# Performance work log

Hardware: AMD Instinct MI355X
Metric: run time of the kernel (lower is better)

The kernel has to match this reference:

```python
import jax, jax.numpy as jnp
import numpy as np

T, N, E = 8, 10000, 200000
F_IN, H, OUT = 32, 128, 64
EPS = 1e-5


def setup_inputs() -> dict:
    key = jax.random.key(0)
    ks = jax.random.split(key, 28)
    inp = {}
    inp['x'] = jax.random.normal(ks[0], (T, N, F_IN), jnp.float32)
    inp['edge_index'] = jax.random.randint(ks[1], (2, E), 0, N, dtype=jnp.int32)
    # GCN layer weights (Glorot-ish scale)
    inp['w_gcn0'] = jax.random.normal(ks[2], (F_IN, H), jnp.float32) / np.float32(np.sqrt(F_IN))
    inp['b_gcn0'] = jnp.zeros((H,), jnp.float32)
    inp['w_gcn1'] = jax.random.normal(ks[3], (H, H), jnp.float32) / np.float32(np.sqrt(H))
    inp['b_gcn1'] = jnp.zeros((H,), jnp.float32)
    inp['w_gcn2'] = jax.random.normal(ks[4], (H, H), jnp.float32) / np.float32(np.sqrt(H))
    inp['b_gcn2'] = jnp.zeros((H,), jnp.float32)
    # BatchNorm (eval mode) params for the two inner norms
    for i, kb in zip(range(2), range(5, 9, 2)):
        inp[f'bn_g{i}'] = 1.0 + 0.1 * jax.random.normal(ks[kb], (H,), jnp.float32)
        inp[f'bn_b{i}'] = 0.1 * jax.random.normal(ks[kb + 1], (H,), jnp.float32)
        inp[f'bn_m{i}'] = 0.1 * jax.random.normal(ks[kb + 10], (H,), jnp.float32)
        inp[f'bn_v{i}'] = jax.random.uniform(ks[kb + 11], (H,), jnp.float32, 0.5, 1.5)
    # 3-layer LSTM params, torch gate order (i, f, g, o)
    s = np.float32(1.0 / np.sqrt(OUT))
    dims_in = [H, OUT, OUT]
    for l in range(3):
        k0, k1, k2, k3 = jax.random.split(ks[20 + l], 4)
        inp[f'w_ih_{l}'] = jax.random.uniform(k0, (4 * OUT, dims_in[l]), jnp.float32, -s, s)
        inp[f'w_hh_{l}'] = jax.random.uniform(k1, (4 * OUT, OUT), jnp.float32, -s, s)
        inp[f'b_ih_{l}'] = jax.random.uniform(k2, (4 * OUT,), jnp.float32, -s, s)
        inp[f'b_hh_{l}'] = jax.random.uniform(k3, (4 * OUT,), jnp.float32, -s, s)
    return inp


def reference(x, edge_index, w_gcn0, b_gcn0, w_gcn1, b_gcn1, w_gcn2, b_gcn2,
              bn_g0, bn_b0, bn_m0, bn_v0, bn_g1, bn_b1, bn_m1, bn_v1,
              w_ih_0, w_hh_0, b_ih_0, b_hh_0,
              w_ih_1, w_hh_1, b_ih_1, b_hh_1,
              w_ih_2, w_hh_2, b_ih_2, b_hh_2):
    src, dst = edge_index[0], edge_index[1]
    # symmetric GCN normalization with self-loops: deg = in-degree + 1
    deg = jax.ops.segment_sum(jnp.ones((E,), x.dtype), dst, num_segments=N) + 1.0
    dis = jax.lax.rsqrt(deg)
    coef = dis[src] * dis[dst]          # [E] edge norm
    self_w = dis * dis                   # [N] self-loop norm

    def gcn(h, W, b):
        hw = jnp.einsum('tnf,fo->tno', h, W)                      # [T,N,O]
        msg = hw[:, src, :] * coef[None, :, None]                  # [T,E,O]
        agg = jax.vmap(lambda m: jax.ops.segment_sum(m, dst, num_segments=N))(msg)
        return agg + hw * self_w[None, :, None] + b

    def bn(h, g, b_, m, v):  # eval-mode BatchNorm1d
        return (h - m) * (g * jax.lax.rsqrt(v + EPS)) + b_

    h = bn(jax.nn.relu(gcn(x, w_gcn0, b_gcn0)), bn_g0, bn_b0, bn_m0, bn_v0)
    h = bn(jax.nn.relu(gcn(h, w_gcn1, b_gcn1)), bn_g1, bn_b1, bn_m1, bn_v1)
    h = jax.nn.relu(gcn(h, w_gcn2, b_gcn2))                        # [T,N,H]

    def lstm_layer(xs, Wih, Whh, bih, bhh):
        Hd = Whh.shape[1]
        bias = bih + bhh
        def step(carry, xt):
            hp, cp = carry
            g = xt @ Wih.T + hp @ Whh.T + bias
            i, f, gg, o = jnp.split(g, 4, axis=-1)
            c = jax.nn.sigmoid(f) * cp + jax.nn.sigmoid(i) * jnp.tanh(gg)
            hn = jax.nn.sigmoid(o) * jnp.tanh(c)
            return (hn, c), hn
        z = jnp.zeros((xs.shape[1], Hd), xs.dtype)
        _, ys = jax.lax.scan(step, (z, z), xs)
        return ys  # [T,N,Hd]

    ys = lstm_layer(h, w_ih_0, w_hh_0, b_ih_0, b_hh_0)
    ys = lstm_layer(ys, w_ih_1, w_hh_1, b_ih_1, b_hh_1)
    ys = lstm_layer(ys, w_ih_2, w_hh_2, b_ih_2, b_hh_2)
    return ys[-1]  # [N, OUT] == x[:, -1, :] in the torch code
```

## Files before the change

kernel.cpp:

```cpp
#include <hip/hip_runtime.h>
#include <hip/hip_bf16.h>
#include <math.h>

#define NTHREADS 256
#define T_STEPS 8
#define F_INC 32
#define H_DIM 128
#define O_DIM 64

typedef unsigned short u16;
typedef __attribute__((ext_vector_type(8))) short short8_t;
typedef __attribute__((ext_vector_type(4))) float float4_t;

__device__ __forceinline__ float bf2f(u16 u) {
    return __uint_as_float(((unsigned)u) << 16);
}
__device__ __forceinline__ u16 f2bf(float f) {
    __hip_bfloat16 h = __float2bfloat16(f);
    union { __hip_bfloat16 h; u16 s; } cv; cv.h = h; return cv.s;
}
__device__ __forceinline__ float4 ld_bf4(const u16* p) {
    uint2 u = *(const uint2*)p;
    return make_float4(__uint_as_float(u.x << 16), __uint_as_float(u.x & 0xffff0000u),
                       __uint_as_float(u.y << 16), __uint_as_float(u.y & 0xffff0000u));
}
__device__ __forceinline__ void st_bf4(u16* p, float4 v) {
    ushort4 s = make_ushort4(f2bf(v.x), f2bf(v.y), f2bf(v.z), f2bf(v.w));
    *(ushort4*)p = s;
}
__device__ __forceinline__ void bf8_unpack(uint4 u, float* f) {
    f[0] = __uint_as_float(u.x << 16); f[1] = __uint_as_float(u.x & 0xffff0000u);
    f[2] = __uint_as_float(u.y << 16); f[3] = __uint_as_float(u.y & 0xffff0000u);
    f[4] = __uint_as_float(u.z << 16); f[5] = __uint_as_float(u.z & 0xffff0000u);
    f[6] = __uint_as_float(u.w << 16); f[7] = __uint_as_float(u.w & 0xffff0000u);
}
__device__ __forceinline__ float fsig(float x) {
    float xc = fminf(fmaxf(x, -30.f), 30.f);
    float e = __builtin_amdgcn_exp2f(xc * -1.4426950408889634f);
    return __builtin_amdgcn_rcpf(1.0f + e);
}
__device__ __forceinline__ float ftanh(float x) {
    float xc = fminf(fmaxf(x, -15.f), 15.f);
    float e = __builtin_amdgcn_exp2f(xc * -2.8853900817779268f);
    float r = __builtin_amdgcn_rcpf(1.0f + e);
    return fmaf(-2.0f * e, r, 1.0f);
}

__global__ void init_cnt_kernel(int* __restrict__ cnt, int n) {
    int i = blockIdx.x * NTHREADS + threadIdx.x;
    if (i < n) cnt[i] = 0;
}

__global__ void count_kernel(const int* __restrict__ ei, int* __restrict__ cnt, int E) {
    int e = blockIdx.x * NTHREADS + threadIdx.x;
    if (e < E) atomicAdd(&cnt[ei[E + e]], 1);
}

__global__ void scan_part1(const int* __restrict__ cnt, int* __restrict__ bsum, int n) {
    __shared__ int sd[NTHREADS];
    const int i = blockIdx.x * NTHREADS + threadIdx.x;
    sd[threadIdx.x] = (i < n) ? cnt[i] : 0;
    __syncthreads();
    for (int off = 128; off > 0; off >>= 1) {
        if (threadIdx.x < off) sd[threadIdx.x] += sd[threadIdx.x + off];
        __syncthreads();
    }
    if (threadIdx.x == 0) bsum[blockIdx.x] = sd[0];
}
__global__ void scan_part2(const int* __restrict__ bsum, int* __restrict__ boff, int nb) {
    if (threadIdx.x == 0) {
        int s = 0;
        for (int b = 0; b < nb; ++b) { boff[b] = s; s += bsum[b]; }
    }
}
__global__ void scan_part3(const int* __restrict__ cnt, const int* __restrict__ boff,
                           int* __restrict__ rowptr, int* __restrict__ wp,
                           float* __restrict__ dis, float* __restrict__ selfw, int n) {
    __shared__ int sd[NTHREADS];
    const int i = blockIdx.x * NTHREADS + threadIdx.x;
    const int v = (i < n) ? cnt[i] : 0;
    sd[threadIdx.x] = v;
    __syncthreads();
    for (int off = 1; off < NTHREADS; off <<= 1) {
        const int tv = (threadIdx.x >= off) ? sd[threadIdx.x - off] : 0;
        __syncthreads();
        sd[threadIdx.x] += tv;
        __syncthreads();
    }
    const int excl = boff[blockIdx.x] + sd[threadIdx.x] - v;
    if (i < n) {
        rowptr[i] = excl; wp[i] = excl;
        if (i == n - 1) rowptr[n] = excl + v;
        const float d = 1.0f + (float)v;
        dis[i] = rsqrtf(d);
        selfw[i] = 1.0f / d;
    }
}

__global__ void fill_kernel(const int* __restrict__ ei, const float* __restrict__ dis,
                            int* __restrict__ wp, int* __restrict__ csr_src,
                            float* __restrict__ coefA, int E) {
    int e = blockIdx.x * NTHREADS + threadIdx.x;
    if (e < E) {
        int s = ei[e], d = ei[E + e];
        int p = atomicAdd(&wp[d], 1);
        csr_src[p] = s;
        coefA[p] = dis[s] * dis[d];
    }
}

__global__ void wprep_all_kernel(const float* g0, const float* g1, const float* g2,
                                 const float* i0, const float* i1, const float* i2,
                                 const float* h0, const float* h1, const float* h2,
                                 u16* o_g0, u16* o_g1, u16* o_g2,
                                 u16* o_i0, u16* o_i1, u16* o_i2,
                                 u16* o_h0, u16* o_h1, u16* o_h2) {
    const int i = blockIdx.x * NTHREADS + threadIdx.x;
    if (i < 4096)        { o_g0[i] = f2bf(g0[(i & 31) * 128 + (i >> 5)]); }
    else if (i < 20480)  { int j = i - 4096;   o_g1[j] = f2bf(g1[(j & 127) * 128 + (j >> 7)]); }
    else if (i < 36864)  { int j = i - 20480;  o_g2[j] = f2bf(g2[(j & 127) * 128 + (j >> 7)]); }
    else if (i < 69632)  { int j = i - 36864;  o_i0[j] = f2bf(i0[j]); }
    else if (i < 86016)  { int j = i - 69632;  o_i1[j] = f2bf(i1[j]); }
    else if (i < 102400) { int j = i - 86016;  o_i2[j] = f2bf(i2[j]); }
    else if (i < 118784) { int j = i - 102400; o_h0[j] = f2bf(h0[j]); }
    else if (i < 135168) { int j = i - 118784; o_h1[j] = f2bf(h1[j]); }
    else if (i < 151552) { int j = i - 135168; o_h2[j] = f2bf(h2[j]); }
}

__global__ __launch_bounds__(NTHREADS)
void agg32t_kernel(const float* __restrict__ x, const int* __restrict__ rowptr,
                   const int* __restrict__ csrc, const float* __restrict__ coefA,
                   const float* __restrict__ selfw, u16* __restrict__ out, int N) {
    const int t = blockIdx.x;
    const int n = blockIdx.y * 4 + (threadIdx.x >> 6);
    const int lane = threadIdx.x & 63;
    const int split = lane >> 3;
    const int c4 = (lane & 7) * 4;
    const float* xb = x + (long)t * N * 32;
    const int e0 = rowptr[n], e1 = rowptr[n + 1];
    float a[4] = {};
    #pragma unroll 2
    for (int e = e0 + split; e < e1; e += 8) {
        const float wgt = coefA[e];
        const int s = csrc[e];
        const float4 v = *(const float4*)(xb + (long)s * 32 + c4);
        a[0] = fmaf(wgt, v.x, a[0]);
        a[1] = fmaf(wgt, v.y, a[1]);
        a[2] = fmaf(wgt, v.z, a[2]);
        a[3] = fmaf(wgt, v.w, a[3]);
    }
    #pragma unroll
    for (int j = 0; j < 4; ++j) {
        a[j] += __shfl_xor(a[j], 8);
        a[j] += __shfl_xor(a[j], 16);
        a[j] += __shfl_xor(a[j], 32);
    }
    if (split == 0) {
        const float sw = selfw[n];
        const float4 sv = *(const float4*)(xb + (long)n * 32 + c4);
        float4 r = make_float4(fmaf(sw, sv.x, a[0]), fmaf(sw, sv.y, a[1]),
                               fmaf(sw, sv.z, a[2]), fmaf(sw, sv.w, a[3]));
        st_bf4(out + ((long)t * N + n) * 32 + c4, r);
    }
}

__global__ __launch_bounds__(NTHREADS)
void agg128t_kernel(const u16* __restrict__ h, const int* __restrict__ rowptr,
                    const int* __restrict__ csrc, const float* __restrict__ coefA,
                    const float* __restrict__ selfw, u16* __restrict__ out, int N) {
    const int t = blockIdx.x;
    const int n = blockIdx.y * 4 + (threadIdx.x >> 6);
    const int lane = threadIdx.x & 63;
    const int split = lane >> 4;
    const int c8 = (lane & 15) * 8;
    const u16* hb = h + (long)t * N * 128;
    const int e0 = rowptr[n], e1 = rowptr[n + 1];
    float a[8] = {};
    #pragma unroll 2
    for (int e = e0 + split; e < e1; e += 4) {
        const float wgt = coefA[e];
        const int s = csrc[e];
        const uint4 v = *(const uint4*)(hb + (long)s * 128 + c8);
        float f[8];
        bf8_unpack(v, f);
        #pragma unroll
        for (int j = 0; j < 8; ++j) a[j] = fmaf(wgt, f[j], a[j]);
    }
    #pragma unroll
    for (int j = 0; j < 8; ++j) {
        a[j] += __shfl_xor(a[j], 16);
        a[j] += __shfl_xor(a[j], 32);
    }
    if (split == 0) {
        const float sw = selfw[n];
        const uint4 sv = *(const uint4*)(hb + (long)n * 128 + c8);
        float f[8];
        bf8_unpack(sv, f);
        ushort4 o0, o1;
        o0.x = f2bf(fmaf(sw, f[0], a[0])); o0.y = f2bf(fmaf(sw, f[1], a[1]));
        o0.z = f2bf(fmaf(sw, f[2], a[2])); o0.w = f2bf(fmaf(sw, f[3], a[3]));
        o1.x = f2bf(fmaf(sw, f[4], a[4])); o1.y = f2bf(fmaf(sw, f[5], a[5]));
        o1.z = f2bf(fmaf(sw, f[6], a[6])); o1.w = f2bf(fmaf(sw, f[7], a[7]));
        u16* op = out + ((long)t * N + n) * 128 + c8;
        *(ushort4*)op = o0;
        *(ushort4*)(op + 4) = o1;
    }
}

template<int K, int EPI, bool OUTBF>
__global__ __launch_bounds__(NTHREADS)
void mfma_gemm_kernel(const u16* __restrict__ A, const u16* __restrict__ Bt,
                      const float* __restrict__ bias0,
                      const float* __restrict__ bng, const float* __restrict__ bnb,
                      const float* __restrict__ bnm, const float* __restrict__ bnv,
                      void* __restrict__ Cout, int ldc) {
    constexpr int KC = (K < 64) ? K : 64;
    constexpr int KP = KC + 8;
    constexpr int KV = KC / 8;
    __shared__ __align__(16) u16 As[128 * KP];
    __shared__ __align__(16) u16 Bs[128 * KP];
    const int tid = threadIdx.x;
    const long row0 = (long)blockIdx.x * 128;
    const int col0 = blockIdx.y * 128;
    const int wid = tid >> 6, lane = tid & 63;
    const int quad = lane >> 4, l16 = lane & 15;

    float4_t acc[2][8];
    #pragma unroll
    for (int rt = 0; rt < 2; ++rt)
        #pragma unroll
        for (int ct = 0; ct < 8; ++ct)
            acc[rt][ct] = (float4_t){0.f, 0.f, 0.f, 0.f};

    const int arow = wid * 32 + l16;
    const int koff = quad * 8;
    for (int ch = 0; ch < K / KC; ++ch) {
        const int kbase = ch * KC;
        for (int p = tid; p < 128 * KV; p += NTHREADS) {
            const int r = p / KV, kv = p % KV;
            *(uint4*)(&As[r * KP + kv * 8]) =
                *(const uint4*)(A + (row0 + r) * K + kbase + kv * 8);
        }
        for (int p = tid; p < 128 * KV; p += NTHREADS) {
            const int r = p / KV, kv = p % KV;
            *(uint4*)(&Bs[r * KP + kv * 8]) =
                *(const uint4*)(Bt + (long)(col0 + r) * K + kbase + kv * 8);
        }
        __syncthreads();
        #pragma unroll
        for (int kc = 0; kc < KC / 32; ++kc) {
            const short8_t a0 = *(const short8_t*)(&As[arow * KP + kc * 32 + koff]);
            const short8_t a1 = *(const short8_t*)(&As[(arow + 16) * KP + kc * 32 + koff]);
            #pragma unroll
            for (int ct = 0; ct < 8; ++ct) {
                const short8_t b = *(const short8_t*)(&Bs[(ct * 16 + l16) * KP + kc * 32 + koff]);
                acc[0][ct] = __builtin_amdgcn_mfma_f32_16x16x32_bf16(a0, b, acc[0][ct], 0, 0, 0);
                acc[1][ct] = __builtin_amdgcn_mfma_f32_16x16x32_bf16(a1, b, acc[1][ct], 0, 0, 0);
            }
        }
        __syncthreads();
    }

    float e_add0[8], e_mul[8], e_add1[8];
    #pragma unroll
    for (int ct = 0; ct < 8; ++ct) {
        const int c = col0 + ct * 16 + l16;
        e_add0[ct] = bias0[c];
        if constexpr (EPI == 2) {
            const float s = bng[c] * rsqrtf(bnv[c] + 1e-5f);
            e_mul[ct] = s;
            e_add1[ct] = bnb[c] - bnm[c] * s;
        }
    }
    #pragma unroll
    for (int rt = 0; rt < 2; ++rt) {
        #pragma unroll
        for (int r = 0; r < 4; ++r) {
            const long row = row0 + wid * 32 + rt * 16 + quad * 4 + r;
            #pragma unroll
            for (int ct = 0; ct < 8; ++ct) {
                float v = fmaxf(acc[rt][ct][r] + e_add0[ct], 0.f);
                if constexpr (EPI == 2) v = fmaf(v, e_mul[ct], e_add1[ct]);
                const long idx = row * (long)ldc + col0 + ct * 16 + l16;
                if constexpr (OUTBF) ((u16*)Cout)[idx] = f2bf(v);
                else ((float*)Cout)[idx] = v;
            }
        }
    }
}

template<int KIN, bool IN_SPLIT, bool LAST>
__global__ __launch_bounds__(NTHREADS, 2)
void lstm_layer_kernel(const u16* __restrict__ in_hi, const u16* __restrict__ in_lo,
                       const u16* __restrict__ wih, const u16* __restrict__ whh,
                       const float* __restrict__ bi, const float* __restrict__ bh,
                       u16* __restrict__ out_hi, u16* __restrict__ out_lo,
                       float* __restrict__ out_f, int N) {
    constexpr int NKS = KIN / 32;
    constexpr int HSTR = 76;
    const int tid = threadIdx.x;
    const int w = tid >> 6, lane = tid & 63;
    const int quad = lane >> 4, l16 = lane & 15;
    const int n0 = blockIdx.x * 16;
    const int u = w * 16 + l16;

    __shared__ __align__(16) u16 hT[2][16][HSTR];
    for (int p = tid; p < 2 * 16 * HSTR; p += NTHREADS) (&hT[0][0][0])[p] = 0;

    short8_t fI[4][NKS], fH[4][2];
    #pragma unroll
    for (int g = 0; g < 4; ++g) {
        #pragma unroll
        for (int ks = 0; ks < NKS; ++ks)
            fI[g][ks] = *(const short8_t*)(wih + (long)(g * 64 + u) * KIN + ks * 32 + quad * 8);
        #pragma unroll
        for (int ks = 0; ks < 2; ++ks)
            fH[g][ks] = *(const short8_t*)(whh + (long)(g * 64 + u) * 64 + ks * 32 + quad * 8);
    }
    float bias[4];
    #pragma unroll
    for (int g = 0; g < 4; ++g) bias[g] = bi[g * 64 + u] + bh[g * 64 + u];
    float cst[4] = {};
    __syncthreads();

    #pragma unroll 1
    for (int t = 0; t < T_STEPS; ++t) {
        short8_t ain[NKS], ainl[NKS];
        const long ibase = ((long)t * N + n0 + l16) * KIN + quad * 8;
        #pragma unroll
        for (int ks = 0; ks < NKS; ++ks) {
            ain[ks] = *(const short8_t*)(in_hi + ibase + ks * 32);
            if constexpr (IN_SPLIT) ainl[ks] = *(const short8_t*)(in_lo + ibase + ks * 32);
        }
        short8_t ah[2], al[2];
        #pragma unroll
        for (int ks = 0; ks < 2; ++ks) {
            ah[ks] = *(const short8_t*)(&hT[0][l16][ks * 32 + quad * 8]);
            al[ks] = *(const short8_t*)(&hT[1][l16][ks * 32 + quad * 8]);
        }
        __syncthreads();

        float4_t acc[4];
        #pragma unroll
        for (int g = 0; g < 4; ++g) acc[g] = (float4_t){bias[g], bias[g], bias[g], bias[g]};
        #pragma unroll
        for (int ks = 0; ks < NKS; ++ks)
            #pragma unroll
            for (int g = 0; g < 4; ++g) {
                acc[g] = __builtin_amdgcn_mfma_f32_16x16x32_bf16(ain[ks], fI[g][ks], acc[g], 0, 0, 0);
                if constexpr (IN_SPLIT)
                    acc[g] = __builtin_amdgcn_mfma_f32_16x16x32_bf16(ainl[ks], fI[g][ks], acc[g], 0, 0, 0);
            }
        #pragma unroll
        for (int ks = 0; ks < 2; ++ks)
            #pragma unroll
            for (int g = 0; g < 4; ++g) {
                acc[g] = __builtin_amdgcn_mfma_f32_16x16x32_bf16(ah[ks], fH[g][ks], acc[g], 0, 0, 0);
                acc[g] = __builtin_amdgcn_mfma_f32_16x16x32_bf16(al[ks], fH[g][ks], acc[g], 0, 0, 0);
            }

        #pragma unroll
        for (int r = 0; r < 4; ++r) {
            const float si = fsig(acc[0][r]);
            const float sf = fsig(acc[1][r]);
            const float gg = ftanh(acc[2][r]);
            const float so = fsig(acc[3][r]);
            const float c = sf * cst[r] + si * gg;
            cst[r] = c;
            const float h = so * ftanh(c);
            const int node = quad * 4 + r;
            const u16 hi = f2bf(h);
            const u16 lo = f2bf(h - bf2f(hi));
            hT[0][node][u] = hi;
            hT[1][node][u] = lo;
            if constexpr (LAST) {
                if (t == T_STEPS - 1) out_f[(long)(n0 + node) * 64 + u] = h;
            } else {
                const long o = ((long)t * N + n0 + node) * 64 + u;
                out_hi[o] = hi;
                out_lo[o] = lo;
            }
        }
        __syncthreads();
    }
}

extern "C" void kernel_launch(void* const* d_in, const int* in_sizes, int n_in,
                              void* d_out, int out_size, void* d_ws, size_t ws_size,
                              hipStream_t stream) {
    (void)n_in; (void)out_size; (void)ws_size;
    const float* x      = (const float*)d_in[0];
    const int*   ei     = (const int*)d_in[1];
    const float* w_gcn0 = (const float*)d_in[2];
    const float* b_gcn0 = (const float*)d_in[3];
    const float* w_gcn1 = (const float*)d_in[4];
    const float* b_gcn1 = (const float*)d_in[5];
    const float* w_gcn2 = (const float*)d_in[6];
    const float* b_gcn2 = (const float*)d_in[7];
    const float* bn_g0  = (const float*)d_in[8];
    const float* bn_b0  = (const float*)d_in[9];
    const float* bn_m0  = (const float*)d_in[10];
    const float* bn_v0  = (const float*)d_in[11];
    const float* bn_g1  = (const float*)d_in[12];
    const float* bn_b1  = (const float*)d_in[13];
    const float* bn_m1  = (const float*)d_in[14];
    const float* bn_v1  = (const float*)d_in[15];
    const float* w_ih_0 = (const float*)d_in[16];
    const float* w_hh_0 = (const float*)d_in[17];
    const float* b_ih_0 = (const float*)d_in[18];
    const float* b_hh_0 = (const float*)d_in[19];
    const float* w_ih_1 = (const float*)d_in[20];
    const float* w_hh_1 = (const float*)d_in[21];
    const float* b_ih_1 = (const float*)d_in[22];
    const float* b_hh_1 = (const float*)d_in[23];
    const float* w_ih_2 = (const float*)d_in[24];
    const float* w_hh_2 = (const float*)d_in[25];
    const float* b_ih_2 = (const float*)d_in[26];
    const float* b_hh_2 = (const float*)d_in[27];

    const int E = in_sizes[1] / 2;
    const int N = in_sizes[0] / (T_STEPS * F_INC);
    const long M = (long)N * T_STEPS;

    char* ws = (char*)d_ws;
    size_t off = 0;
    auto carve = [&](size_t bytes) -> void* {
        void* p = ws + off;
        off += (bytes + 255) & ~(size_t)255;
        return p;
    };
    float* dis     = (float*)carve((size_t)N * 4);
    float* selfw   = (float*)carve((size_t)N * 4);
    float* coefA   = (float*)carve((size_t)E * 4);
    int*   cnt     = (int*)carve((size_t)N * 4);
    int*   rowptr  = (int*)carve((size_t)(N + 1) * 4);
    int*   wp      = (int*)carve((size_t)N * 4);
    int*   csr_src = (int*)carve((size_t)E * 4);
    int*   bsum    = (int*)carve(64 * 4);
    int*   boff    = (int*)carve(64 * 4);
    u16*   hbuf    = (u16*)carve((size_t)M * H_DIM * 2);
    u16*   abuf    = (u16*)carve((size_t)M * H_DIM * 2);
    u16*   pA_hi   = (u16*)carve((size_t)M * O_DIM * 2);
    u16*   pA_lo   = (u16*)carve((size_t)M * O_DIM * 2);
    u16*   pB_hi   = (u16*)carve((size_t)M * O_DIM * 2);
    u16*   pB_lo   = (u16*)carve((size_t)M * O_DIM * 2);
    u16*   wt0     = (u16*)carve((size_t)128 * 32 * 2);
    u16*   wt1     = (u16*)carve((size_t)128 * 128 * 2);
    u16*   wt2     = (u16*)carve((size_t)128 * 128 * 2);
    u16*   wtih0   = (u16*)carve((size_t)256 * 128 * 2);
    u16*   wtih1   = (u16*)carve((size_t)256 * 64 * 2);
    u16*   wtih2   = (u16*)carve((size_t)256 * 64 * 2);
    u16*   whh0b   = (u16*)carve((size_t)256 * 64 * 2);
    u16*   whh1b   = (u16*)carve((size_t)256 * 64 * 2);
    u16*   whh2b   = (u16*)carve((size_t)256 * 64 * 2);

    const dim3 b256(NTHREADS);
    const int gN = (N + NTHREADS - 1) / NTHREADS;
    const int gE = (E + NTHREADS - 1) / NTHREADS;

    init_cnt_kernel<<<gN, b256, 0, stream>>>(cnt, N);
    count_kernel<<<gE, b256, 0, stream>>>(ei, cnt, E);
    scan_part1<<<gN, b256, 0, stream>>>(cnt, bsum, N);
    scan_part2<<<1, 64, 0, stream>>>(bsum, boff, gN);
    scan_part3<<<gN, b256, 0, stream>>>(cnt, boff, rowptr, wp, dis, selfw, N);
    fill_kernel<<<gE, b256, 0, stream>>>(ei, dis, wp, csr_src, coefA, E);

    wprep_all_kernel<<<(151552 + 255) / 256, b256, 0, stream>>>(
        w_gcn0, w_gcn1, w_gcn2, w_ih_0, w_ih_1, w_ih_2, w_hh_0, w_hh_1, w_hh_2,
        wt0, wt1, wt2, wtih0, wtih1, wtih2, whh0b, whh1b, whh2b);

    const int gBlk = (int)(M / 128);
    agg32t_kernel<<<dim3(T_STEPS, N / 4), b256, 0, stream>>>(
        x, rowptr, csr_src, coefA, selfw, abuf, N);
    mfma_gemm_kernel<32, 2, true><<<dim3(gBlk, 1), b256, 0, stream>>>(
        abuf, wt0, b_gcn0, bn_g0, bn_b0, bn_m0, bn_v0, hbuf, 128);
    agg128t_kernel<<<dim3(T_STEPS, N / 4), b256, 0, stream>>>(
        hbuf, rowptr, csr_src, coefA, selfw, abuf, N);
    mfma_gemm_kernel<128, 2, true><<<dim3(gBlk, 1), b256, 0, stream>>>(
        abuf, wt1, b_gcn1, bn_g1, bn_b1, bn_m1, bn_v1, hbuf, 128);
    agg128t_kernel<<<dim3(T_STEPS, N / 4), b256, 0, stream>>>(
        hbuf, rowptr, csr_src, coefA, selfw, abuf, N);
    mfma_gemm_kernel<128, 1, true><<<dim3(gBlk, 1), b256, 0, stream>>>(
        abuf, wt2, b_gcn2, nullptr, nullptr, nullptr, nullptr, hbuf, 128);

    const int gL = N / 16;
    lstm_layer_kernel<128, false, false><<<gL, b256, 0, stream>>>(
        hbuf, nullptr, wtih0, whh0b, b_ih_0, b_hh_0, pA_hi, pA_lo, nullptr, N);
    lstm_layer_kernel<64, true, false><<<gL, b256, 0, stream>>>(
        pA_hi, pA_lo, wtih1, whh1b, b_ih_1, b_hh_1, pB_hi, pB_lo, nullptr, N);
    lstm_layer_kernel<64, true, true><<<gL, b256, 0, stream>>>(
        pB_hi, pB_lo, wtih2, whh2b, b_ih_2, b_hh_2, nullptr, nullptr, (float*)d_out, N);
}
```

Measured before the change: 377.6 us.

## Fuse GCN aggregation with MFMA transform and drop separate scan pass

Each GCN layer's neighbour aggregation and its dense weight transform (with bias, ReLU and BatchNorm epilogue) now run in one kernel. A block aggregates 16 nodes into shared memory and then multiplies that tile by the weights with MFMA. This removes the intermediate aggregation buffer round trip and three kernel launches. The single-thread scan_part2 is folded into scan_part3 via a wavefront reduction, and the count init becomes a memset. In exchange, each block now rereads the weights from global memory with a very small 16-row tile, and the aggregation loop is serialized to four nodes per wave.

```diff
diff --git a/kernel.cpp b/kernel.cpp
--- a/kernel.cpp
+++ b/kernel.cpp
@@ -19,15 +19,6 @@
     __hip_bfloat16 h = __float2bfloat16(f);
     union { __hip_bfloat16 h; u16 s; } cv; cv.h = h; return cv.s;
 }
-__device__ __forceinline__ float4 ld_bf4(const u16* p) {
-    uint2 u = *(const uint2*)p;
-    return make_float4(__uint_as_float(u.x << 16), __uint_as_float(u.x & 0xffff0000u),
-                       __uint_as_float(u.y << 16), __uint_as_float(u.y & 0xffff0000u));
-}
-__device__ __forceinline__ void st_bf4(u16* p, float4 v) {
-    ushort4 s = make_ushort4(f2bf(v.x), f2bf(v.y), f2bf(v.z), f2bf(v.w));
-    *(ushort4*)p = s;
-}
 __device__ __forceinline__ void bf8_unpack(uint4 u, float* f) {
     f[0] = __uint_as_float(u.x << 16); f[1] = __uint_as_float(u.x & 0xffff0000u);
     f[2] = __uint_as_float(u.y << 16); f[3] = __uint_as_float(u.y & 0xffff0000u);
@@ -44,11 +35,6 @@
     float e = __builtin_amdgcn_exp2f(xc * -2.8853900817779268f);
     float r = __builtin_amdgcn_rcpf(1.0f + e);
     return fmaf(-2.0f * e, r, 1.0f);
-}
-
-__global__ void init_cnt_kernel(int* __restrict__ cnt, int n) {
-    int i = blockIdx.x * NTHREADS + threadIdx.x;
-    if (i < n) cnt[i] = 0;
 }
 
 __global__ void count_kernel(const int* __restrict__ ei, int* __restrict__ cnt, int E) {
@@ -67,27 +53,30 @@
     }
     if (threadIdx.x == 0) bsum[blockIdx.x] = sd[0];
 }
-__global__ void scan_part2(const int* __restrict__ bsum, int* __restrict__ boff, int nb) {
-    if (threadIdx.x == 0) {
-        int s = 0;
-        for (int b = 0; b < nb; ++b) { boff[b] = s; s += bsum[b]; }
-    }
-}
-__global__ void scan_part3(const int* __restrict__ cnt, const int* __restrict__ boff,
+
+__global__ void scan_part3(const int* __restrict__ cnt, const int* __restrict__ bsum,
                            int* __restrict__ rowptr, int* __restrict__ wp,
                            float* __restrict__ dis, float* __restrict__ selfw, int n) {
     __shared__ int sd[NTHREADS];
-    const int i = blockIdx.x * NTHREADS + threadIdx.x;
+    __shared__ int sbase;
+    const int tid = threadIdx.x;
+    if (tid < 64) {
+        int v0 = (tid < blockIdx.x) ? bsum[tid] : 0;
+        #pragma unroll
+        for (int off = 1; off < 64; off <<= 1) v0 += __shfl_xor(v0, off);
+        if (tid == 0) sbase = v0;
+    }
+    const int i = blockIdx.x * NTHREADS + tid;
     const int v = (i < n) ? cnt[i] : 0;
-    sd[threadIdx.x] = v;
+    sd[tid] = v;
     __syncthreads();
     for (int off = 1; off < NTHREADS; off <<= 1) {
-        const int tv = (threadIdx.x >= off) ? sd[threadIdx.x - off] : 0;
+        const int tv = (tid >= off) ? sd[tid - off] : 0;
         __syncthreads();
-        sd[threadIdx.x] += tv;
+        sd[tid] += tv;
         __syncthreads();
     }
-    const int excl = boff[blockIdx.x] + sd[threadIdx.x] - v;
+    const int excl = sbase + sd[tid] - v;
     if (i < n) {
         rowptr[i] = excl; wp[i] = excl;
         if (i == n - 1) rowptr[n] = excl + v;
@@ -128,163 +117,172 @@
 }
 
 __global__ __launch_bounds__(NTHREADS)
-void agg32t_kernel(const float* __restrict__ x, const int* __restrict__ rowptr,
-                   const int* __restrict__ csrc, const float* __restrict__ coefA,
-                   const float* __restrict__ selfw, u16* __restrict__ out, int N) {
+void gcn32_kernel(const float* __restrict__ x, const int* __restrict__ rowptr,
+                  const int* __restrict__ csrc, const float* __restrict__ coefA,
+                  const float* __restrict__ selfw, const u16* __restrict__ Wt,
+                  const float* __restrict__ bias,
+                  const float* __restrict__ bng, const float* __restrict__ bnb,
+                  const float* __restrict__ bnm, const float* __restrict__ bnv,
+                  u16* __restrict__ out, int N) {
+    constexpr int ASTR = 40;
+    __shared__ __align__(16) u16 aT[16][ASTR];
     const int t = blockIdx.x;
-    const int n = blockIdx.y * 4 + (threadIdx.x >> 6);
-    const int lane = threadIdx.x & 63;
+    const int n0 = blockIdx.y * 16;
+    const int tid = threadIdx.x;
+    const int wid = tid >> 6, lane = tid & 63;
+    const int quad = lane >> 4, l16 = lane & 15;
+    const float* xb = x + (long)t * N * 32;
+
     const int split = lane >> 3;
     const int c4 = (lane & 7) * 4;
-    const float* xb = x + (long)t * N * 32;
-    const int e0 = rowptr[n], e1 = rowptr[n + 1];
-    float a[4] = {};
-    #pragma unroll 2
-    for (int e = e0 + split; e < e1; e += 8) {
-        const float wgt = coefA[e];
-        const int s = csrc[e];
-        const float4 v = *(const float4*)(xb + (long)s * 32 + c4);
-        a[0] = fmaf(wgt, v.x, a[0]);
-        a[1] = fmaf(wgt, v.y, a[1]);
-        a[2] = fmaf(wgt, v.z, a[2]);
-        a[3] = fmaf(wgt, v.w, a[3]);
-    }
-    #pragma unroll
-    for (int j = 0; j < 4; ++j) {
-        a[j] += __shfl_xor(a[j], 8);
-        a[j] += __shfl_xor(a[j], 16);
-        a[j] += __shfl_xor(a[j], 32);
-    }
-    if (split == 0) {
-        const float sw = selfw[n];
-        const float4 sv = *(const float4*)(xb + (long)n * 32 + c4);
-        float4 r = make_float4(fmaf(sw, sv.x, a[0]), fmaf(sw, sv.y, a[1]),
-                               fmaf(sw, sv.z, a[2]), fmaf(sw, sv.w, a[3]));
-        st_bf4(out + ((long)t * N + n) * 32 + c4, r);
-    }
-}
-
+    for (int i = 0; i < 4; ++i) {
+        const int n = n0 + wid * 4 + i;
+        const int e0 = rowptr[n], e1 = rowptr[n + 1];
+        float a[4] = {};
+        #pragma unroll 2
+        for (int e = e0 + split; e < e1; e += 8) {
+            const float wgt = coefA[e];
+            const int s = csrc[e];
+            const float4 v = *(const float4*)(xb + (long)s * 32 + c4);
+            a[0] = fmaf(wgt, v.x, a[0]);
+            a[1] = fmaf(wgt, v.y, a[1]);
+            a[2] = fmaf(wgt, v.z, a[2]);
+            a[3] = fmaf(wgt, v.w, a[3]);
+        }
+        #pragma unroll
+        for (int j = 0; j < 4; ++j) {
+            a[j] += __shfl_xor(a[j], 8);
+            a[j] += __shfl_xor(a[j], 16);
+            a[j] += __shfl_xor(a[j], 32);
+        }
+        if (split == 0) {
+            const float sw = selfw[n];
+            const float4 sv = *(const float4*)(xb + (long)n * 32 + c4);
+            ushort4 o;
+            o.x = f2bf(fmaf(sw, sv.x, a[0]));
+            o.y = f2bf(fmaf(sw, sv.y, a[1]));
+            o.z = f2bf(fmaf(sw, sv.z, a[2]));
+            o.w = f2bf(fmaf(sw, sv.w, a[3]));
+            *(ushort4*)(&aT[wid * 4 + i][c4]) = o;
+        }
+    }
+    __syncthreads();
+
+    const short8_t fA = *(const short8_t*)(&aT[l16][quad * 8]);
+    float4_t acc[2];
+    short8_t fB[2];
+    #pragma unroll
+    for (int ct = 0; ct < 2; ++ct) {
+        const int col = wid * 32 + ct * 16 + l16;
+        fB[ct] = *(const short8_t*)(Wt + (long)col * 32 + quad * 8);
+        acc[ct] = (float4_t){0.f, 0.f, 0.f, 0.f};
+    }
+    #pragma unroll
+    for (int ct = 0; ct < 2; ++ct)
+        acc[ct] = __builtin_amdgcn_mfma_f32_16x16x32_bf16(fA, fB[ct], acc[ct], 0, 0, 0);
+
+    #pragma unroll
+    for (int ct = 0; ct < 2; ++ct) {
+        const int c = wid * 32 + ct * 16 + l16;
+        const float s = bng[c] * rsqrtf(bnv[c] + 1e-5f);
+        const float a1 = bnb[c] - bnm[c] * s;
+        const float a0 = bias[c];
+        #pragma unroll
+        for (int r = 0; r < 4; ++r) {
+            const int node = quad * 4 + r;
+            float v = fmaf(fmaxf(acc[ct][r] + a0, 0.f), s, a1);
+            out[((long)t * N + n0 + node) * 128 + c] = f2bf(v);
+        }
+    }
+}
+
+template<int EPI>
 __global__ __launch_bounds__(NTHREADS)
-void agg128t_kernel(const u16* __restrict__ h, const int* __restrict__ rowptr,
-                    const int* __restrict__ csrc, const float* __restrict__ coefA,
-                    const float* __restrict__ selfw, u16* __restrict__ out, int N) {
+void gcn128_kernel(const u16* __restrict__ h, const int* __restrict__ rowptr,
+                   const int* __restrict__ csrc, const float* __restrict__ coefA,
+                   const float* __restrict__ selfw, const u16* __restrict__ Wt,
+                   const float* __restrict__ bias,
+                   const float* __restrict__ bng, const float* __restrict__ bnb,
+                   const float* __restrict__ bnm, const float* __restrict__ bnv,
+                   u16* __restrict__ out, int N) {
+    constexpr int ASTR = 136;
+    __shared__ __align__(16) u16 aT[16][ASTR];
     const int t = blockIdx.x;
-    const int n = blockIdx.y * 4 + (threadIdx.x >> 6);
-    const int lane = threadIdx.x & 63;
-    const int split = lane >> 4;
-    const int c8 = (lane & 15) * 8;
-    const u16* hb = h + (long)t * N * 128;
-    const int e0 = rowptr[n], e1 = rowptr[n + 1];
-    float a[8] = {};
-    #pragma unroll 2
-    for (int e = e0 + split; e < e1; e += 4) {
-        const float wgt = coefA[e];
-        const int s = csrc[e];
-        const uint4 v = *(const uint4*)(hb + (long)s * 128 + c8);
-        float f[8];
-        bf8_unpack(v, f);
-        #pragma unroll
-        for (int j = 0; j < 8; ++j) a[j] = fmaf(wgt, f[j], a[j]);
-    }
-    #pragma unroll
-    for (int j = 0; j < 8; ++j) {
-        a[j] += __shfl_xor(a[j], 16);
-        a[j] += __shfl_xor(a[j], 32);
-    }
-    if (split == 0) {
-        const float sw = selfw[n];
-        const uint4 sv = *(const uint4*)(hb + (long)n * 128 + c8);
-        float f[8];
-        bf8_unpack(sv, f);
-        ushort4 o0, o1;
-        o0.x = f2bf(fmaf(sw, f[0], a[0])); o0.y = f2bf(fmaf(sw, f[1], a[1]));
-        o0.z = f2bf(fmaf(sw, f[2], a[2])); o0.w = f2bf(fmaf(sw, f[3], a[3]));
-        o1.x = f2bf(fmaf(sw, f[4], a[4])); o1.y = f2bf(fmaf(sw, f[5], a[5]));
-        o1.z = f2bf(fmaf(sw, f[6], a[6])); o1.w = f2bf(fmaf(sw, f[7], a[7]));
-        u16* op = out + ((long)t * N + n) * 128 + c8;
-        *(ushort4*)op = o0;
-        *(ushort4*)(op + 4) = o1;
-    }
-}
-
-template<int K, int EPI, bool OUTBF>
-__global__ __launch_bounds__(NTHREADS)
-void mfma_gemm_kernel(const u16* __restrict__ A, const u16* __restrict__ Bt,
-                      const float* __restrict__ bias0,
-                      const float* __restrict__ bng, const float* __restrict__ bnb,
-                      const float* __restrict__ bnm, const float* __restrict__ bnv,
-                      void* __restrict__ Cout, int ldc) {
-    constexpr int KC = (K < 64) ? K : 64;
-    constexpr int KP = KC + 8;
-    constexpr int KV = KC / 8;
-    __shared__ __align__(16) u16 As[128 * KP];
-    __shared__ __align__(16) u16 Bs[128 * KP];
+    const int n0 = blockIdx.y * 16;
     const int tid = threadIdx.x;
-    const long row0 = (long)blockIdx.x * 128;
-    const int col0 = blockIdx.y * 128;
     const int wid = tid >> 6, lane = tid & 63;
     const int quad = lane >> 4, l16 = lane & 15;
-
-    float4_t acc[2][8];
-    #pragma unroll
-    for (int rt = 0; rt < 2; ++rt)
-        #pragma unroll
-        for (int ct = 0; ct < 8; ++ct)
-            acc[rt][ct] = (float4_t){0.f, 0.f, 0.f, 0.f};
-
-    const int arow = wid * 32 + l16;
-    const int koff = quad * 8;
-    for (int ch = 0; ch < K / KC; ++ch) {
-        const int kbase = ch * KC;
-        for (int p = tid; p < 128 * KV; p += NTHREADS) {
-            const int r = p / KV, kv = p % KV;
-            *(uint4*)(&As[r * KP + kv * 8]) =
-                *(const uint4*)(A + (row0 + r) * K + kbase + kv * 8);
-        }
-        for (int p = tid; p < 128 * KV; p += NTHREADS) {
-            const int r = p / KV, kv = p % KV;
-            *(uint4*)(&Bs[r * KP + kv * 8]) =
-                *(const uint4*)(Bt + (long)(col0 + r) * K + kbase + kv * 8);
-        }
-        __syncthreads();
-        #pragma unroll
-        for (int kc = 0; kc < KC / 32; ++kc) {
-            const short8_t a0 = *(const short8_t*)(&As[arow * KP + kc * 32 + koff]);
-            const short8_t a1 = *(const short8_t*)(&As[(arow + 16) * KP + kc * 32 + koff]);
+    const u16* hb = h + (long)t * N * 128;
+
+    const int split = lane >> 4;
+    const int c8 = l16 * 8;
+    for (int i = 0; i < 4; ++i) {
+        const int n = n0 + wid * 4 + i;
+        const int e0 = rowptr[n], e1 = rowptr[n + 1];
+        float a[8] = {};
+        #pragma unroll 2
+        for (int e = e0 + split; e < e1; e += 4) {
+            const float wgt = coefA[e];
+            const int s = csrc[e];
+            const uint4 v = *(const uint4*)(hb + (long)s * 128 + c8);
+            float f[8];
+            bf8_unpack(v, f);
             #pragma unroll
-            for (int ct = 0; ct < 8; ++ct) {
-                const short8_t b = *(const short8_t*)(&Bs[(ct * 16 + l16) * KP + kc * 32 + koff]);
-                acc[0][ct] = __builtin_amdgcn_mfma_f32_16x16x32_bf16(a0, b, acc[0][ct], 0, 0, 0);
-                acc[1][ct] = __builtin_amdgcn_mfma_f32_16x16x32_bf16(a1, b, acc[1][ct], 0, 0, 0);
-            }
-        }
-        __syncthreads();
-    }
-
-    float e_add0[8], e_mul[8], e_add1[8];
-    #pragma unroll
-    for (int ct = 0; ct < 8; ++ct) {
-        const int c = col0 + ct * 16 + l16;
-        e_add0[ct] = bias0[c];
+            for (int j = 0; j < 8; ++j) a[j] = fmaf(wgt, f[j], a[j]);
+        }
+        #pragma unroll
+        for (int j = 0; j < 8; ++j) {
+            a[j] += __shfl_xor(a[j], 16);
+            a[j] += __shfl_xor(a[j], 32);
+        }
+        if (split == 0) {
+            const float sw = selfw[n];
+            const uint4 sv = *(const uint4*)(hb + (long)n * 128 + c8);
+            float f[8];
+            bf8_unpack(sv, f);
+            ushort4 o0, o1;
+            o0.x = f2bf(fmaf(sw, f[0], a[0])); o0.y = f2bf(fmaf(sw, f[1], a[1]));
+            o0.z = f2bf(fmaf(sw, f[2], a[2])); o0.w = f2bf(fmaf(sw, f[3], a[3]));
+            o1.x = f2bf(fmaf(sw, f[4], a[4])); o1.y = f2bf(fmaf(sw, f[5], a[5]));
+            o1.z = f2bf(fmaf(sw, f[6], a[6])); o1.w = f2bf(fmaf(sw, f[7], a[7]));
+            *(ushort4*)(&aT[wid * 4 + i][c8]) = o0;
+            *(ushort4*)(&aT[wid * 4 + i][c8 + 4]) = o1;
+        }
+    }
+    __syncthreads();
+
+    short8_t fA[4];
+    #pragma unroll
+    for (int ks = 0; ks < 4; ++ks)
+        fA[ks] = *(const short8_t*)(&aT[l16][ks * 32 + quad * 8]);
+    float4_t acc[2];
+    #pragma unroll
+    for (int ct = 0; ct < 2; ++ct) acc[ct] = (float4_t){0.f, 0.f, 0.f, 0.f};
+    #pragma unroll
+    for (int ct = 0; ct < 2; ++ct) {
+        const int col = wid * 32 + ct * 16 + l16;
+        #pragma unroll
+        for (int ks = 0; ks < 4; ++ks) {
+            const short8_t fB = *(const short8_t*)(Wt + (long)col * 128 + ks * 32 + quad * 8);
+            acc[ct] = __builtin_amdgcn_mfma_f32_16x16x32_bf16(fA[ks], fB, acc[ct], 0, 0, 0);
+        }
+    }
+
+    #pragma unroll
+    for (int ct = 0; ct < 2; ++ct) {
+        const int c = wid * 32 + ct * 16 + l16;
+        const float a0 = bias[c];
+        float s = 0.f, a1 = 0.f;
         if constexpr (EPI == 2) {
-            const float s = bng[c] * rsqrtf(bnv[c] + 1e-5f);
-            e_mul[ct] = s;
-            e_add1[ct] = bnb[c] - bnm[c] * s;
-        }
-    }
-    #pragma unroll
-    for (int rt = 0; rt < 2; ++rt) {
+            s = bng[c] * rsqrtf(bnv[c] + 1e-5f);
+            a1 = bnb[c] - bnm[c] * s;
+        }
         #pragma unroll
         for (int r = 0; r < 4; ++r) {
-            const long row = row0 + wid * 32 + rt * 16 + quad * 4 + r;
-            #pragma unroll
-            for (int ct = 0; ct < 8; ++ct) {
-                float v = fmaxf(acc[rt][ct][r] + e_add0[ct], 0.f);
-                if constexpr (EPI == 2) v = fmaf(v, e_mul[ct], e_add1[ct]);
-                const long idx = row * (long)ldc + col0 + ct * 16 + l16;
-                if constexpr (OUTBF) ((u16*)Cout)[idx] = f2bf(v);
-                else ((float*)Cout)[idx] = v;
-            }
+            const int node = quad * 4 + r;
+            float v = fmaxf(acc[ct][r] + a0, 0.f);
+            if constexpr (EPI == 2) v = fmaf(v, s, a1);
+            out[((long)t * N + n0 + node) * 128 + c] = f2bf(v);
         }
     }
 }
@@ -437,9 +435,8 @@
     int*   wp      = (int*)carve((size_t)N * 4);
     int*   csr_src = (int*)carve((size_t)E * 4);
     int*   bsum    = (int*)carve(64 * 4);
-    int*   boff    = (int*)carve(64 * 4);
     u16*   hbuf    = (u16*)carve((size_t)M * H_DIM * 2);
-    u16*   abuf    = (u16*)carve((size_t)M * H_DIM * 2);
+    u16*   hbuf2   = (u16*)carve((size_t)M * H_DIM * 2);
     u16*   pA_hi   = (u16*)carve((size_t)M * O_DIM * 2);
     u16*   pA_lo   = (u16*)carve((size_t)M * O_DIM * 2);
     u16*   pB_hi   = (u16*)carve((size_t)M * O_DIM * 2);
@@ -458,30 +455,26 @@
     const int gN = (N + NTHREADS - 1) / NTHREADS;
     const int gE = (E + NTHREADS - 1) / NTHREADS;
 
-    init_cnt_kernel<<<gN, b256, 0, stream>>>(cnt, N);
+    hipMemsetAsync(cnt, 0, (size_t)N * 4, stream);
     count_kernel<<<gE, b256, 0, stream>>>(ei, cnt, E);
     scan_part1<<<gN, b256, 0, stream>>>(cnt, bsum, N);
-    scan_part2<<<1, 64, 0, stream>>>(bsum, boff, gN);
-    scan_part3<<<gN, b256, 0, stream>>>(cnt, boff, rowptr, wp, dis, selfw, N);
+    scan_part3<<<gN, b256, 0, stream>>>(cnt, bsum, rowptr, wp, dis, selfw, N);
     fill_kernel<<<gE, b256, 0, stream>>>(ei, dis, wp, csr_src, coefA, E);
 
     wprep_all_kernel<<<(151552 + 255) / 256, b256, 0, stream>>>(
         w_gcn0, w_gcn1, w_gcn2, w_ih_0, w_ih_1, w_ih_2, w_hh_0, w_hh_1, w_hh_2,
         wt0, wt1, wt2, wtih0, wtih1, wtih2, whh0b, whh1b, whh2b);
 
-    const int gBlk = (int)(M / 128);
-    agg32t_kernel<<<dim3(T_STEPS, N / 4), b256, 0, stream>>>(
-        x, rowptr, csr_src, coefA, selfw, abuf, N);
-    mfma_gemm_kernel<32, 2, true><<<dim3(gBlk, 1), b256, 0, stream>>>(
-        abuf, wt0, b_gcn0, bn_g0, bn_b0, bn_m0, bn_v0, hbuf, 128);
-    agg128t_kernel<<<dim3(T_STEPS, N / 4), b256, 0, stream>>>(
-        hbuf, rowptr, csr_src, coefA, selfw, abuf, N);
-    mfma_gemm_kernel<128, 2, true><<<dim3(gBlk, 1), b256, 0, stream>>>(
-        abuf, wt1, b_gcn1, bn_g1, bn_b1, bn_m1, bn_v1, hbuf, 128);
-    agg128t_kernel<<<dim3(T_STEPS, N / 4), b256, 0, stream>>>(
-        hbuf, rowptr, csr_src, coefA, selfw, abuf, N);
-    mfma_gemm_kernel<128, 1, true><<<dim3(gBlk, 1), b256, 0, stream>>>(
-        abuf, wt2, b_gcn2, nullptr, nullptr, nullptr, nullptr, hbuf, 128);
+    const dim3 gG(T_STEPS, N / 16);
+    gcn32_kernel<<<gG, b256, 0, stream>>>(
+        x, rowptr, csr_src, coefA, selfw, wt0, b_gcn0,
+        bn_g0, bn_b0, bn_m0, bn_v0, hbuf, N);
+    gcn128_kernel<2><<<gG, b256, 0, stream>>>(
+        hbuf, rowptr, csr_src, coefA, selfw, wt1, b_gcn1,
+        bn_g1, bn_b1, bn_m1, bn_v1, hbuf2, N);
+    gcn128_kernel<1><<<gG, b256, 0, stream>>>(
+        hbuf2, rowptr, csr_src, coefA, selfw, wt2, b_gcn2,
+        nullptr, nullptr, nullptr, nullptr, hbuf, N);
 
     const int gL = N / 16;
     lstm_layer_kernel<128, false, false><<<gL, b256, 0, stream>>>(
```

After: 370.4 us. About the same (-1.9%).
